# Kernel optimization log

Measured on AMD Instinct MI355X. Metric: run time of the kernel, lower is better.

## Reference

```python
import jax, jax.numpy as jnp
import numpy as np

D_IN, D, H, NL, DFF = 128, 256, 4, 4, 1024
N, B, L = 32768, 64, 672


def setup_inputs() -> dict:
    key = jax.random.key(0)
    ks = jax.random.split(key, 12)
    s = 0.02
    return {
        "dom_embeddings": jax.random.normal(ks[0], (N, D_IN), jnp.float32),
        "dom_to_event_idx": jax.random.randint(ks[1], (N,), 0, B, jnp.int32),
        "batch_size": B,
        "seq_len": L,
        "proj_w": jax.random.normal(ks[2], (D_IN, D), jnp.float32) * s,
        "proj_b": jnp.zeros((D,), jnp.float32),
        "cls_token": jax.random.normal(ks[3], (D,), jnp.float32),
        "ln1_g": jnp.ones((NL, D), jnp.float32),
        "ln1_b": jnp.zeros((NL, D), jnp.float32),
        "qkv_w": jax.random.normal(ks[4], (NL, D, 3 * D), jnp.float32) * s,
        "qkv_b": jnp.zeros((NL, 3 * D), jnp.float32),
        "out_w": jax.random.normal(ks[5], (NL, D, D), jnp.float32) * s,
        "out_b": jnp.zeros((NL, D), jnp.float32),
        "ln2_g": jnp.ones((NL, D), jnp.float32),
        "ln2_b": jnp.zeros((NL, D), jnp.float32),
        "ff1_w": jax.random.normal(ks[6], (NL, D, DFF), jnp.float32) * s,
        "ff1_b": jnp.zeros((NL, DFF), jnp.float32),
        "ff2_w": jax.random.normal(ks[7], (NL, DFF, D), jnp.float32) * s,
        "ff2_b": jnp.zeros((NL, D), jnp.float32),
        "head1_w": jax.random.normal(ks[8], (D, D), jnp.float32) * s,
        "head1_b": jnp.zeros((D,), jnp.float32),
        "head2_w": jax.random.normal(ks[9], (D, 3), jnp.float32) * s,
        "head2_b": jnp.zeros((3,), jnp.float32),
    }


def _ln(x, g, b):
    m = jnp.mean(x, axis=-1, keepdims=True)
    v = jnp.var(x, axis=-1, keepdims=True)
    return (x - m) / jnp.sqrt(v + 1e-5) * g + b


def _forward(dom_embeddings, proj_w, proj_b, cls_token, ln1_g, ln1_b, qkv_w, qkv_b,
             out_w, out_b, ln2_g, ln2_b, ff1_w, ff1_b, ff2_w, ff2_b,
             head1_w, head1_b, head2_w, head2_b, idx, batch_size, seq_len):
    n = idx.shape[0]
    d = proj_w.shape[1]
    dh = d // H
    x = dom_embeddings @ proj_w + proj_b  # (N, d)

    # per-segment rank (replaces the python for-loop): stable argsort + cumsum of counts
    counts = jnp.zeros((batch_size,), jnp.int32).at[idx].add(1)
    starts = jnp.cumsum(counts) - counts
    order = jnp.argsort(idx)  # jax sort is stable -> preserves in-event order
    rank_sorted = jnp.arange(n, dtype=jnp.int32) - starts[idx[order]]
    positions = jnp.zeros((n,), jnp.int32).at[order].set(rank_sorted)

    # scatter into padded batch; slot 0 is cls (note: cls KEY stays masked, as in torch code)
    bt = jnp.zeros((batch_size, seq_len, d), x.dtype).at[:, 0, :].set(cls_token)
    bt = bt.at[idx, positions + 1].set(x)
    pad = jnp.ones((batch_size, seq_len), bool).at[idx, positions + 1].set(False)
    bias = jnp.where(pad, -jnp.inf, 0.0).astype(x.dtype)[:, None, None, :]  # (B,1,1,L)

    h = bt
    for i in range(NL):  # norm_first pre-LN encoder layers
        y = _ln(h, ln1_g[i], ln1_b[i])
        qkv = y @ qkv_w[i] + qkv_b[i]
        q, k, v = jnp.split(qkv, 3, axis=-1)
        q = q.reshape(batch_size, seq_len, H, dh)
        k = k.reshape(batch_size, seq_len, H, dh)
        v = v.reshape(batch_size, seq_len, H, dh)
        scores = jnp.einsum('bqhd,bkhd->bhqk', q, k) * (1.0 / np.sqrt(dh))
        attn = jax.nn.softmax(scores + bias, axis=-1)
        o = jnp.einsum('bhqk,bkhd->bqhd', attn, v).reshape(batch_size, seq_len, d)
        h = h + o @ out_w[i] + out_b[i]
        z = _ln(h, ln2_g[i], ln2_b[i])
        h = h + jax.nn.relu(z @ ff1_w[i] + ff1_b[i]) @ ff2_w[i] + ff2_b[i]

    cls = h[:, 0, :]
    p = jax.nn.relu(cls @ head1_w + head1_b) @ head2_w + head2_b
    return p / jnp.sqrt(jnp.sum(p * p, axis=1, keepdims=True))


def reference(dom_embeddings, dom_to_event_idx, batch_size, seq_len, proj_w, proj_b,
              cls_token, ln1_g, ln1_b, qkv_w, qkv_b, out_w, out_b, ln2_g, ln2_b,
              ff1_w, ff1_b, ff2_w, ff2_b, head1_w, head1_b, head2_w, head2_b):
    return _forward(dom_embeddings, proj_w, proj_b, cls_token, ln1_g, ln1_b, qkv_w,
                    qkv_b, out_w, out_b, ln2_g, ln2_b, ff1_w, ff1_b, ff2_w, ff2_b,
                    head1_w, head1_b, head2_w, head2_b,
                    dom_to_event_idx, batch_size, seq_len)
```

## Files before the change

kernel.cpp:

```cpp
#include <hip/hip_runtime.h>
#include <cstdint>
#include <cstddef>

#define NDOM   32768
#define DIN    128
#define DMODEL 256
#define NHEAD  4
#define NLAYER 4
#define DFFN   1024
#define BATCH  64
#define SEQ    672
#define DHEAD  64
#define MROWS  (BATCH*SEQ)

typedef unsigned short u16;
typedef __attribute__((ext_vector_type(8))) short bf8;
typedef __attribute__((ext_vector_type(4))) float f4;

__device__ inline u16 f2b(float x) {
    union { float f; unsigned u; } c; c.f = x;
    unsigned r = c.u + 0x7fffu + ((c.u >> 16) & 1u);
    return (u16)(r >> 16);
}

__device__ inline void gload16(const void* g, const void* l) {
    __builtin_amdgcn_global_load_lds(
        (const __attribute__((address_space(1))) void*)g,
        (__attribute__((address_space(3))) void*)l, 16, 0, 0);
}


__global__ void k_zero_counts(int* __restrict__ counts) {
    if (threadIdx.x < BATCH) counts[threadIdx.x] = 0;
}

__global__ void k_pos(const int* __restrict__ idx, int* __restrict__ counts,
                      int* __restrict__ pos) {
    int i = blockIdx.x * blockDim.x + threadIdx.x;
    if (i < NDOM) pos[i] = atomicAdd(&counts[idx[i]], 1);
}

__global__ void k_init_h(float* __restrict__ h, const float* __restrict__ cls) {
    const float4* cls4 = (const float4*)cls;
    float4* h4 = (float4*)h;
    const int total4 = MROWS * DMODEL / 4;
    for (int f = blockIdx.x * blockDim.x + threadIdx.x; f < total4;
         f += gridDim.x * blockDim.x) {
        int d4 = f & 63;
        int t  = (f >> 6) % SEQ;
        h4[f] = (t == 0) ? cls4[d4] : make_float4(0.f, 0.f, 0.f, 0.f);
    }
}

__global__ void k_b16(const float* __restrict__ x, u16* __restrict__ y, int n4) {
    int i = blockIdx.x * 256 + threadIdx.x;
    if (i < n4) {
        float4 v = ((const float4*)x)[i];
        ushort4 o;
        o.x = f2b(v.x); o.y = f2b(v.y); o.z = f2b(v.z); o.w = f2b(v.w);
        ((ushort4*)y)[i] = o;
    }
}

__global__ __launch_bounds__(256) void k_wt_all(
    const float* __restrict__ projw, const float* __restrict__ qkvw,
    const float* __restrict__ outw,  const float* __restrict__ ff1w,
    const float* __restrict__ ff2w,
    u16* __restrict__ wpj, u16* __restrict__ wq, u16* __restrict__ wo,
    u16* __restrict__ w1,  u16* __restrict__ w2)
{
    __shared__ float t[64][65];
    const int tile = blockIdx.x;
    const float* W; u16* D; int K, N, local;
    if (tile < 8)        { W = projw; D = wpj; K = 128;  N = 256;  local = tile; }
    else if (tile < 200) { int l = (tile-8)/48;   local = (tile-8)%48;
                           W = qkvw + (size_t)l*196608; D = wq + (size_t)l*196608; K = 256;  N = 768; }
    else if (tile < 264) { int l = (tile-200)/16; local = (tile-200)%16;
                           W = outw + (size_t)l*65536;  D = wo + (size_t)l*65536;  K = 256;  N = 256; }
    else if (tile < 520) { int l = (tile-264)/64; local = (tile-264)%64;
                           W = ff1w + (size_t)l*262144; D = w1 + (size_t)l*262144; K = 256;  N = 1024; }
    else                 { int l = (tile-520)/64; local = (tile-520)%64;
                           W = ff2w + (size_t)l*262144; D = w2 + (size_t)l*262144; K = 1024; N = 256; }
    const int ntn = N >> 6;
    const int tk = local / ntn, tn = local % ntn;
    const int r = threadIdx.x >> 6, c = threadIdx.x & 63;
    #pragma unroll 4
    for (int rr = r; rr < 64; rr += 4)
        t[rr][c] = W[(size_t)(tk*64 + rr) * N + tn*64 + c];
    __syncthreads();
    #pragma unroll 4
    for (int rr = r; rr < 64; rr += 4)
        D[(size_t)(tn*64 + rr) * K + tk*64 + c] = f2b(t[c][rr]);
}

__global__ __launch_bounds__(256) void k_scatter(
    const float* __restrict__ xp, const int* __restrict__ idx,
    const int* __restrict__ pos, float* __restrict__ h)
{
    const int i = blockIdx.x * 4 + (threadIdx.x >> 6);
    const int lane = threadIdx.x & 63;
    const int p = pos[i] + 1;
    if (p >= SEQ) return;
    const size_t row = (size_t)idx[i] * SEQ + p;
    ((float4*)(h + row * DMODEL))[lane] = ((const float4*)(xp + (size_t)i * DMODEL))[lane];
}


__global__ __launch_bounds__(256) void k_ln_bf(
    const float* __restrict__ x, const float* __restrict__ g,
    const float* __restrict__ bt, u16* __restrict__ y)
{
    const int row  = blockIdx.x * 4 + (threadIdx.x >> 6);
    const int lane = threadIdx.x & 63;
    float4 v = ((const float4*)(x + (size_t)row * DMODEL))[lane];
    float s = v.x + v.y + v.z + v.w;
    #pragma unroll
    for (int off = 32; off >= 1; off >>= 1) s += __shfl_xor(s, off);
    const float m = s * (1.f / DMODEL);
    const float d0 = v.x - m, d1 = v.y - m, d2 = v.z - m, d3 = v.w - m;
    float q = d0*d0 + d1*d1 + d2*d2 + d3*d3;
    #pragma unroll
    for (int off = 32; off >= 1; off >>= 1) q += __shfl_xor(q, off);
    const float rstd = rsqrtf(q * (1.f / DMODEL) + 1e-5f);
    const float4 gv = ((const float4*)g)[lane];
    const float4 bv = ((const float4*)bt)[lane];
    ushort4 o;
    o.x = f2b(d0 * rstd * gv.x + bv.x);
    o.y = f2b(d1 * rstd * gv.y + bv.y);
    o.z = f2b(d2 * rstd * gv.z + bv.z);
    o.w = f2b(d3 * rstd * gv.w + bv.w);
    ((ushort4*)(y + (size_t)row * DMODEL))[lane] = o;
}


template<int RELU, int RESID, int OBF, int OF32>
__global__ __launch_bounds__(256) void k_gemm_bf(
    const u16* __restrict__ A, const u16* __restrict__ Bt,
    const float* __restrict__ bias, float* __restrict__ Cf,
    u16* __restrict__ Cb, int K, int N)
{
    __shared__ u16 As[8192];
    __shared__ u16 Bs[8192];
    const int tid = threadIdx.x;
    const int w = tid >> 6, lane = tid & 63;
    const int lr = lane & 15, lg = lane >> 4;
    const int m0 = blockIdx.y * 128, n0 = blockIdx.x * 128;
    const int wm = (w >> 1) * 64, wn = (w & 1) * 64;

    const f4 zf = {0.f, 0.f, 0.f, 0.f};
    f4 acc[4][4];
    #pragma unroll
    for (int i = 0; i < 4; ++i)
        #pragma unroll
        for (int j = 0; j < 4; ++j) acc[i][j] = zf;

    const int srow8 = lane >> 3;
    const int sq = lane & 7;

    for (int k0 = 0; k0 < K; k0 += 64) {
        #pragma unroll
        for (int c = 0; c < 4; ++c) {
            const int chunk = w * 4 + c;
            const int row = chunk * 8 + srow8;
            const int ks = k0 + ((sq ^ (row & 7)) << 3);
            gload16(A  + (size_t)(m0 + row) * K + ks, (const char*)As + chunk * 1024);
            gload16(Bt + (size_t)(n0 + row) * K + ks, (const char*)Bs + chunk * 1024);
        }
        __syncthreads();
        #pragma unroll
        for (int kk = 0; kk < 2; ++kk) {
            bf8 af[4], bg[4];
            #pragma unroll
            for (int f = 0; f < 4; ++f) {
                const int ra = wm + f * 16 + lr;
                af[f] = *(const bf8*)((const char*)As + ra * 128 +
                        ((((kk << 2) | lg) ^ (ra & 7)) << 4));
                const int rb = wn + f * 16 + lr;
                bg[f] = *(const bf8*)((const char*)Bs + rb * 128 +
                        ((((kk << 2) | lg) ^ (rb & 7)) << 4));
            }
            #pragma unroll
            for (int fm = 0; fm < 4; ++fm)
                #pragma unroll
                for (int fn = 0; fn < 4; ++fn)
                    acc[fm][fn] = __builtin_amdgcn_mfma_f32_16x16x32_bf16(
                        af[fm], bg[fn], acc[fm][fn], 0, 0, 0);
        }
        __syncthreads();
    }

    float bv[4];
    #pragma unroll
    for (int fn = 0; fn < 4; ++fn) bv[fn] = bias[n0 + wn + fn * 16 + lr];
    #pragma unroll
    for (int fm = 0; fm < 4; ++fm)
        #pragma unroll
        for (int j = 0; j < 4; ++j) {
            const int row = m0 + wm + fm * 16 + lg * 4 + j;
            #pragma unroll
            for (int fn = 0; fn < 4; ++fn) {
                float v = acc[fm][fn][j] + bv[fn];
                if (RELU) v = fmaxf(v, 0.f);
                const size_t off = (size_t)row * N + n0 + wn + fn * 16 + lr;
                if (RESID) Cf[off] += v;
                if (OF32)  Cf[off] = v;
                if (OBF)   Cb[off] = f2b(v);
            }
        }
}


__global__ __launch_bounds__(256) void k_attn_mfma(
    const u16* __restrict__ qkv, const int* __restrict__ counts,
    u16* __restrict__ out)
{
    __shared__ u16 Ks[4096];
    __shared__ u16 Vt[4096];
    __shared__ u16 Ps[4][1024];
    const int tid = threadIdx.x;
    const int w = tid >> 6, lane = tid & 63;
    const int lr = lane & 15, lg = lane >> 4;
    const int b = blockIdx.z, hh = blockIdx.y;
    const int q0 = blockIdx.x * 64;
    const int kmax = min(counts[b], SEQ - 1);
    if (q0 > kmax) return;
    const int ntiles = (kmax + 64) >> 6;
    const size_t bb = (size_t)b * SEQ;

    const int qrow = q0 + w * 16 + lr;
    const size_t qoff = (bb + (size_t)min(qrow, SEQ - 1)) * 768 + hh * 64 + (lg << 3);
    const bf8 qf0 = *(const bf8*)(qkv + qoff);
    const bf8 qf1 = *(const bf8*)(qkv + qoff + 32);

    const f4 zf = {0.f, 0.f, 0.f, 0.f};
    f4 o_[4];
    #pragma unroll
    for (int fn = 0; fn < 4; ++fn) o_[fn] = zf;
    float mrow = -INFINITY, ssum = 0.f;

    for (int kt = 0; kt < ntiles; ++kt) {
        const int k0 = kt * 64;
        #pragma unroll
        for (int c = 0; c < 2; ++c) {
            const int chunk = w * 2 + c;
            const int row = chunk * 8 + (lane >> 3);
            const int q = lane & 7;
            const int krow = min(k0 + row, SEQ - 1);
            gload16(qkv + (bb + krow) * 768 + 256 + hh * 64 + ((q ^ (row & 7)) << 3),
                    (const char*)Ks + chunk * 1024);
        }
        {
            const int kk2 = (tid & 31) * 2;
            const int dh0 = (tid >> 5) * 8;
            const int r0 = min(k0 + kk2, SEQ - 1), r1 = min(k0 + kk2 + 1, SEQ - 1);
            const bf8 v0 = *(const bf8*)(qkv + (bb + r0) * 768 + 512 + hh * 64 + dh0);
            const bf8 v1 = *(const bf8*)(qkv + (bb + r1) * 768 + 512 + hh * 64 + dh0);
            #pragma unroll
            for (int e = 0; e < 8; ++e) {
                const int d = dh0 + e;
                const unsigned pk = (unsigned)(u16)v0[e] | ((unsigned)(u16)v1[e] << 16);
                *(unsigned*)((char*)Vt + d * 128 +
                    ((((kk2 >> 3) ^ (d & 7)) << 4)) + ((kk2 & 7) << 1)) = pk;
            }
        }
        __syncthreads();

        f4 sf[4];
        #pragma unroll
        for (int fk = 0; fk < 4; ++fk) sf[fk] = zf;
        #pragma unroll
        for (int kk = 0; kk < 2; ++kk) {
            const bf8 qf = kk ? qf1 : qf0;
            #pragma unroll
            for (int fk = 0; fk < 4; ++fk) {
                const int rk = fk * 16 + lr;
                const bf8 kf = *(const bf8*)((const char*)Ks + rk * 128 +
                        ((((kk << 2) | lg) ^ (rk & 7)) << 4));
                sf[fk] = __builtin_amdgcn_mfma_f32_16x16x32_bf16(kf, qf, sf[fk], 0, 0, 0);
            }
        }

        float sv[4][4];
        float pmax = -INFINITY;
        #pragma unroll
        for (int fk = 0; fk < 4; ++fk)
            #pragma unroll
            for (int j = 0; j < 4; ++j) {
                const int key = k0 + fk * 16 + lg * 4 + j;
                float x = (key >= 1 && key <= kmax) ? sf[fk][j] * 0.125f : -INFINITY;
                sv[fk][j] = x;
                pmax = fmaxf(pmax, x);
            }
        pmax = fmaxf(pmax, __shfl_xor(pmax, 16));
        pmax = fmaxf(pmax, __shfl_xor(pmax, 32));
        const float mnew = fmaxf(mrow, pmax);
        const float fac = __expf(mrow - mnew);
        mrow = mnew;
        float tsum = 0.f;
        #pragma unroll
        for (int fk = 0; fk < 4; ++fk) {
            const float p0 = __expf(sv[fk][0] - mnew);
            const float p1 = __expf(sv[fk][1] - mnew);
            const float p2 = __expf(sv[fk][2] - mnew);
            const float p3 = __expf(sv[fk][3] - mnew);
            tsum += p0 + p1 + p2 + p3;
            ushort4 pk;
            pk.x = f2b(p0); pk.y = f2b(p1); pk.z = f2b(p2); pk.w = f2b(p3);
            *(ushort4*)((char*)Ps[w] + lr * 128 +
                (((((fk << 1) | (lg >> 1)) ^ (lr & 7)) << 4)) + ((lg & 1) << 3)) = pk;
        }
        tsum += __shfl_xor(tsum, 16);
        tsum += __shfl_xor(tsum, 32);
        ssum = ssum * fac + tsum;

        #pragma unroll
        for (int j = 0; j < 4; ++j) {
            const float fj = __shfl(fac, lg * 4 + j);
            #pragma unroll
            for (int fn = 0; fn < 4; ++fn) o_[fn][j] *= fj;
        }
        __syncthreads();

        #pragma unroll
        for (int kk = 0; kk < 2; ++kk) {
            const bf8 pa = *(const bf8*)((const char*)Ps[w] + lr * 128 +
                    ((((kk << 2) | lg) ^ (lr & 7)) << 4));
            #pragma unroll
            for (int fn = 0; fn < 4; ++fn) {
                const int rv = fn * 16 + lr;
                const bf8 vf = *(const bf8*)((const char*)Vt + rv * 128 +
                        ((((kk << 2) | lg) ^ (rv & 7)) << 4));
                o_[fn] = __builtin_amdgcn_mfma_f32_16x16x32_bf16(pa, vf, o_[fn], 0, 0, 0);
            }
        }
        __syncthreads();
    }

    const float inv = 1.f / ssum;
    #pragma unroll
    for (int j = 0; j < 4; ++j) {
        const float ij = __shfl(inv, lg * 4 + j);
        const int qr = q0 + w * 16 + lg * 4 + j;
        if (qr < SEQ) {
            #pragma unroll
            for (int fn = 0; fn < 4; ++fn)
                out[(bb + qr) * DMODEL + hh * 64 + fn * 16 + lr] = f2b(o_[fn][j] * ij);
        }
    }
}


__global__ __launch_bounds__(256) void k_head(
    const float* __restrict__ h, const float* __restrict__ w1,
    const float* __restrict__ b1, const float* __restrict__ w2,
    const float* __restrict__ b2, float* __restrict__ out)
{
    __shared__ float cbuf[DMODEL];
    __shared__ float p1[DMODEL];
    __shared__ float p2[3];
    const int b = blockIdx.x, tid = threadIdx.x;
    cbuf[tid] = h[(size_t)b * SEQ * DMODEL + tid];
    __syncthreads();
    float acc = b1[tid];
    #pragma unroll 8
    for (int k = 0; k < DMODEL; ++k) acc = fmaf(cbuf[k], w1[k * DMODEL + tid], acc);
    p1[tid] = fmaxf(acc, 0.f);
    __syncthreads();
    if (tid < 3) {
        float a = b2[tid];
        for (int k = 0; k < DMODEL; ++k) a = fmaf(p1[k], w2[k * 3 + tid], a);
        p2[tid] = a;
    }
    __syncthreads();
    if (tid < 3) {
        float n2 = p2[0]*p2[0] + p2[1]*p2[1] + p2[2]*p2[2];
        out[b * 3 + tid] = p2[tid] * rsqrtf(n2);
    }
}


extern "C" void kernel_launch(void* const* d_in, const int* in_sizes, int n_in,
                              void* d_out, int out_size, void* d_ws, size_t ws_size,
                              hipStream_t stream) {
    const float* emb   = (const float*)d_in[0];
    const int*   idx   = (const int*)d_in[1];
    const float* projw = (const float*)d_in[4];
    const float* projb = (const float*)d_in[5];
    const float* cls   = (const float*)d_in[6];
    const float* ln1g  = (const float*)d_in[7];
    const float* ln1b  = (const float*)d_in[8];
    const float* qkvw  = (const float*)d_in[9];
    const float* qkvb  = (const float*)d_in[10];
    const float* outw  = (const float*)d_in[11];
    const float* outb  = (const float*)d_in[12];
    const float* ln2g  = (const float*)d_in[13];
    const float* ln2b  = (const float*)d_in[14];
    const float* ff1w  = (const float*)d_in[15];
    const float* ff1b  = (const float*)d_in[16];
    const float* ff2w  = (const float*)d_in[17];
    const float* ff2b  = (const float*)d_in[18];
    const float* h1w   = (const float*)d_in[19];
    const float* h1b   = (const float*)d_in[20];
    const float* h2w   = (const float*)d_in[21];
    const float* h2b   = (const float*)d_in[22];
    float* out = (float*)d_out;

    char* ws = (char*)d_ws;
    int*   counts = (int*)ws;
    int*   pos    = (int*)(ws + 4096);
    float* h      = (float*)(ws + 135168);
    u16*   ybf    = (u16*)(ws + 44175360);
    u16*   qkvb16 = (u16*)(ws + 66195456);
    u16*   ffb    = (u16*)(ws + 132354048);
    u16*   wq     = (u16*)(ws + 220434432);
    u16*   wo     = (u16*)(ws + 222007296);
    u16*   w1     = (u16*)(ws + 222531584);
    u16*   w2     = (u16*)(ws + 224628736);
    u16*   wpj    = (u16*)(ws + 226725888);
    u16*   embbf  = qkvb16;
    float* xp     = (float*)ffb;

    k_zero_counts<<<1, 64, 0, stream>>>(counts);
    k_pos<<<NDOM / 256, 256, 0, stream>>>(idx, counts, pos);
    k_b16<<<(NDOM * DIN / 4) / 256, 256, 0, stream>>>(emb, embbf, NDOM * DIN / 4);
    k_wt_all<<<776, 256, 0, stream>>>(projw, qkvw, outw, ff1w, ff2w,
                                      wpj, wq, wo, w1, w2);
    k_init_h<<<2688, 256, 0, stream>>>(h, cls);
    k_gemm_bf<0,0,0,1><<<dim3(2, 256), 256, 0, stream>>>(
        embbf, wpj, projb, xp, nullptr, DIN, DMODEL);
    k_scatter<<<NDOM / 4, 256, 0, stream>>>(xp, idx, pos, h);

    for (int l = 0; l < NLAYER; ++l) {
        k_ln_bf<<<MROWS / 4, 256, 0, stream>>>(h, ln1g + l * DMODEL, ln1b + l * DMODEL, ybf);
        k_gemm_bf<0,0,1,0><<<dim3(6, 336), 256, 0, stream>>>(
            ybf, wq + (size_t)l * 196608, qkvb + l * 768, nullptr, qkvb16, 256, 768);
        k_attn_mfma<<<dim3(11, NHEAD, BATCH), 256, 0, stream>>>(qkvb16, counts, ybf);
        k_gemm_bf<0,1,0,0><<<dim3(2, 336), 256, 0, stream>>>(
            ybf, wo + (size_t)l * 65536, outb + l * DMODEL, h, nullptr, 256, 256);
        k_ln_bf<<<MROWS / 4, 256, 0, stream>>>(h, ln2g + l * DMODEL, ln2b + l * DMODEL, ybf);
        k_gemm_bf<1,0,1,0><<<dim3(8, 336), 256, 0, stream>>>(
            ybf, w1 + (size_t)l * 262144, ff1b + l * DFFN, nullptr, ffb, 256, 1024);
        k_gemm_bf<0,1,0,0><<<dim3(2, 336), 256, 0, stream>>>(
            ffb, w2 + (size_t)l * 262144, ff2b + l * DMODEL, h, nullptr, 1024, 256);
    }

    k_head<<<BATCH, 256, 0, stream>>>(h, h1w, h1b, h2w, h2b, out);
}
```

Measured before the change: 1.166 ms.

## Fuse residual GEMMs with following LayerNorm and retile attention to 128-query blocks

Adds a full-row (128x256) GEMM kernel that applies the bias and residual add and then computes the next LayerNorm in its epilogue, writing both h and the bf16 normalized input. This removes the separate LN kernels and their extra reads of h. Attention now uses 512-thread blocks covering 128 queries, with a flattened grid remapped so batches interleave across blocks. It also adds a fast path that skips masking on fully valid key tiles. The risks are lower occupancy, since each full-row block is large and uses more shared memory, and fewer, larger GEMM blocks.

Result: no change. 1.184 ms (+1.6%).

```diff
diff --git a/kernel.cpp b/kernel.cpp
--- a/kernel.cpp
+++ b/kernel.cpp
@@ -210,18 +210,163 @@
 }
 
 
-__global__ __launch_bounds__(256) void k_attn_mfma(
+template<int LNF>
+__global__ __launch_bounds__(512) void k_gemm_ln(
+    const u16* __restrict__ A, const u16* __restrict__ Bt,
+    const float* __restrict__ bias, float* __restrict__ h,
+    u16* __restrict__ ybf, const float* __restrict__ lng,
+    const float* __restrict__ lnb, int K)
+{
+    __shared__ u16 As[8192];
+    __shared__ u16 Bs[16384];
+    __shared__ float red[8][136];
+    const int tid = threadIdx.x;
+    const int w = tid >> 6, lane = tid & 63;
+    const int lr = lane & 15, lg = lane >> 4;
+    const int m0 = blockIdx.x * 128;
+    const int wm = (w >> 2) * 64, wn = (w & 3) * 64;
+
+    const f4 zf = {0.f, 0.f, 0.f, 0.f};
+    f4 acc[4][4];
+    #pragma unroll
+    for (int i = 0; i < 4; ++i)
+        #pragma unroll
+        for (int j = 0; j < 4; ++j) acc[i][j] = zf;
+
+    const int srow8 = lane >> 3;
+    const int sq = lane & 7;
+
+    for (int k0 = 0; k0 < K; k0 += 64) {
+        #pragma unroll
+        for (int c = 0; c < 2; ++c) {
+            const int chunk = w * 2 + c;
+            const int row = chunk * 8 + srow8;
+            const int ks = k0 + ((sq ^ (row & 7)) << 3);
+            gload16(A + (size_t)(m0 + row) * K + ks, (const char*)As + chunk * 1024);
+        }
+        #pragma unroll
+        for (int c = 0; c < 4; ++c) {
+            const int chunk = w * 4 + c;
+            const int row = chunk * 8 + srow8;
+            const int ks = k0 + ((sq ^ (row & 7)) << 3);
+            gload16(Bt + (size_t)row * K + ks, (const char*)Bs + chunk * 1024);
+        }
+        __syncthreads();
+        #pragma unroll
+        for (int kk = 0; kk < 2; ++kk) {
+            bf8 af[4], bg[4];
+            #pragma unroll
+            for (int f = 0; f < 4; ++f) {
+                const int ra = wm + f * 16 + lr;
+                af[f] = *(const bf8*)((const char*)As + ra * 128 +
+                        ((((kk << 2) | lg) ^ (ra & 7)) << 4));
+                const int rb = wn + f * 16 + lr;
+                bg[f] = *(const bf8*)((const char*)Bs + rb * 128 +
+                        ((((kk << 2) | lg) ^ (rb & 7)) << 4));
+            }
+            #pragma unroll
+            for (int fm = 0; fm < 4; ++fm)
+                #pragma unroll
+                for (int fn = 0; fn < 4; ++fn)
+                    acc[fm][fn] = __builtin_amdgcn_mfma_f32_16x16x32_bf16(
+                        af[fm], bg[fn], acc[fm][fn], 0, 0, 0);
+        }
+        __syncthreads();
+    }
+
+    float bv[4];
+    #pragma unroll
+    for (int fn = 0; fn < 4; ++fn) bv[fn] = bias[wn + fn * 16 + lr];
+    float sr[4][4], s2r[4][4];
+    #pragma unroll
+    for (int fm = 0; fm < 4; ++fm)
+        #pragma unroll
+        for (int j = 0; j < 4; ++j) {
+            const int row = m0 + wm + fm * 16 + lg * 4 + j;
+            float s = 0.f, s2 = 0.f;
+            #pragma unroll
+            for (int fn = 0; fn < 4; ++fn) {
+                float v = acc[fm][fn][j] + bv[fn];
+                v += h[(size_t)row * DMODEL + wn + fn * 16 + lr];
+                acc[fm][fn][j] = v;
+                s += v; s2 += v * v;
+            }
+            if (LNF) {
+                #pragma unroll
+                for (int off = 1; off <= 8; off <<= 1) {
+                    s  += __shfl_xor(s, off);
+                    s2 += __shfl_xor(s2, off);
+                }
+            }
+            sr[fm][j] = s; s2r[fm][j] = s2;
+        }
+
+    if (LNF) {
+        if (lr == 0) {
+            #pragma unroll
+            for (int fm = 0; fm < 4; ++fm)
+                #pragma unroll
+                for (int j = 0; j < 4; ++j) {
+                    const int rL = wm + fm * 16 + lg * 4 + j;
+                    red[(w & 3) * 2 + 0][rL] = sr[fm][j];
+                    red[(w & 3) * 2 + 1][rL] = s2r[fm][j];
+                }
+        }
+        __syncthreads();
+        float gl[4], bl[4];
+        #pragma unroll
+        for (int fn = 0; fn < 4; ++fn) {
+            gl[fn] = lng[wn + fn * 16 + lr];
+            bl[fn] = lnb[wn + fn * 16 + lr];
+        }
+        #pragma unroll
+        for (int fm = 0; fm < 4; ++fm)
+            #pragma unroll
+            for (int j = 0; j < 4; ++j) {
+                const int rL = wm + fm * 16 + lg * 4 + j;
+                const int row = m0 + rL;
+                const float S  = red[0][rL] + red[2][rL] + red[4][rL] + red[6][rL];
+                const float S2 = red[1][rL] + red[3][rL] + red[5][rL] + red[7][rL];
+                const float mean = S * (1.f / DMODEL);
+                const float var  = S2 * (1.f / DMODEL) - mean * mean;
+                const float rstd = rsqrtf(var + 1e-5f);
+                #pragma unroll
+                for (int fn = 0; fn < 4; ++fn) {
+                    const float v = acc[fm][fn][j];
+                    const size_t off = (size_t)row * DMODEL + wn + fn * 16 + lr;
+                    h[off] = v;
+                    ybf[off] = f2b((v - mean) * rstd * gl[fn] + bl[fn]);
+                }
+            }
+    } else {
+        #pragma unroll
+        for (int fm = 0; fm < 4; ++fm)
+            #pragma unroll
+            for (int j = 0; j < 4; ++j) {
+                const int row = m0 + wm + fm * 16 + lg * 4 + j;
+                #pragma unroll
+                for (int fn = 0; fn < 4; ++fn)
+                    h[(size_t)row * DMODEL + wn + fn * 16 + lr] = acc[fm][fn][j];
+            }
+    }
+}
+
+
+__global__ __launch_bounds__(512) void k_attn_mfma(
     const u16* __restrict__ qkv, const int* __restrict__ counts,
     u16* __restrict__ out)
 {
     __shared__ u16 Ks[4096];
     __shared__ u16 Vt[4096];
-    __shared__ u16 Ps[4][1024];
+    __shared__ u16 Ps[8][1024];
     const int tid = threadIdx.x;
     const int w = tid >> 6, lane = tid & 63;
     const int lr = lane & 15, lg = lane >> 4;
-    const int b = blockIdx.z, hh = blockIdx.y;
-    const int q0 = blockIdx.x * 64;
+    const int L = blockIdx.x;
+    const int b = (L & 7) * 8 + (L >> 3) / 24;
+    const int r = (L >> 3) % 24;
+    const int qt = r >> 2, hh = r & 3;
+    const int q0 = qt * 128;
     const int kmax = min(counts[b], SEQ - 1);
     if (q0 > kmax) return;
     const int ntiles = (kmax + 64) >> 6;
@@ -240,25 +385,25 @@
 
     for (int kt = 0; kt < ntiles; ++kt) {
         const int k0 = kt * 64;
-        #pragma unroll
-        for (int c = 0; c < 2; ++c) {
-            const int chunk = w * 2 + c;
-            const int row = chunk * 8 + (lane >> 3);
+        {
+            const int row = w * 8 + (lane >> 3);
             const int q = lane & 7;
             const int krow = min(k0 + row, SEQ - 1);
             gload16(qkv + (bb + krow) * 768 + 256 + hh * 64 + ((q ^ (row & 7)) << 3),
-                    (const char*)Ks + chunk * 1024);
+                    (const char*)Ks + w * 1024);
         }
         {
             const int kk2 = (tid & 31) * 2;
-            const int dh0 = (tid >> 5) * 8;
+            const int dh0 = (tid >> 5) * 4;
             const int r0 = min(k0 + kk2, SEQ - 1), r1 = min(k0 + kk2 + 1, SEQ - 1);
-            const bf8 v0 = *(const bf8*)(qkv + (bb + r0) * 768 + 512 + hh * 64 + dh0);
-            const bf8 v1 = *(const bf8*)(qkv + (bb + r1) * 768 + 512 + hh * 64 + dh0);
-            #pragma unroll
-            for (int e = 0; e < 8; ++e) {
+            const ushort4 v0 = *(const ushort4*)(qkv + (bb + r0) * 768 + 512 + hh * 64 + dh0);
+            const ushort4 v1 = *(const ushort4*)(qkv + (bb + r1) * 768 + 512 + hh * 64 + dh0);
+            const u16* pv0 = (const u16*)&v0;
+            const u16* pv1 = (const u16*)&v1;
+            #pragma unroll
+            for (int e = 0; e < 4; ++e) {
                 const int d = dh0 + e;
-                const unsigned pk = (unsigned)(u16)v0[e] | ((unsigned)(u16)v1[e] << 16);
+                const unsigned pk = (unsigned)pv0[e] | ((unsigned)pv1[e] << 16);
                 *(unsigned*)((char*)Vt + d * 128 +
                     ((((kk2 >> 3) ^ (d & 7)) << 4)) + ((kk2 & 7) << 1)) = pk;
             }
@@ -282,15 +427,26 @@
 
         float sv[4][4];
         float pmax = -INFINITY;
-        #pragma unroll
-        for (int fk = 0; fk < 4; ++fk)
-            #pragma unroll
-            for (int j = 0; j < 4; ++j) {
-                const int key = k0 + fk * 16 + lg * 4 + j;
-                float x = (key >= 1 && key <= kmax) ? sf[fk][j] * 0.125f : -INFINITY;
-                sv[fk][j] = x;
-                pmax = fmaxf(pmax, x);
-            }
+        if (k0 >= 1 && k0 + 63 <= kmax) {
+            #pragma unroll
+            for (int fk = 0; fk < 4; ++fk)
+                #pragma unroll
+                for (int j = 0; j < 4; ++j) {
+                    const float x = sf[fk][j] * 0.125f;
+                    sv[fk][j] = x;
+                    pmax = fmaxf(pmax, x);
+                }
+        } else {
+            #pragma unroll
+            for (int fk = 0; fk < 4; ++fk)
+                #pragma unroll
+                for (int j = 0; j < 4; ++j) {
+                    const int key = k0 + fk * 16 + lg * 4 + j;
+                    const float x = (key >= 1 && key <= kmax) ? sf[fk][j] * 0.125f : -INFINITY;
+                    sv[fk][j] = x;
+                    pmax = fmaxf(pmax, x);
+                }
+        }
         pmax = fmaxf(pmax, __shfl_xor(pmax, 16));
         pmax = fmaxf(pmax, __shfl_xor(pmax, 32));
         const float mnew = fmaxf(mrow, pmax);
@@ -429,19 +585,25 @@
     k_gemm_bf<0,0,0,1><<<dim3(2, 256), 256, 0, stream>>>(
         embbf, wpj, projb, xp, nullptr, DIN, DMODEL);
     k_scatter<<<NDOM / 4, 256, 0, stream>>>(xp, idx, pos, h);
+    k_ln_bf<<<MROWS / 4, 256, 0, stream>>>(h, ln1g, ln1b, ybf);
 
     for (int l = 0; l < NLAYER; ++l) {
-        k_ln_bf<<<MROWS / 4, 256, 0, stream>>>(h, ln1g + l * DMODEL, ln1b + l * DMODEL, ybf);
         k_gemm_bf<0,0,1,0><<<dim3(6, 336), 256, 0, stream>>>(
             ybf, wq + (size_t)l * 196608, qkvb + l * 768, nullptr, qkvb16, 256, 768);
-        k_attn_mfma<<<dim3(11, NHEAD, BATCH), 256, 0, stream>>>(qkvb16, counts, ybf);
-        k_gemm_bf<0,1,0,0><<<dim3(2, 336), 256, 0, stream>>>(
-            ybf, wo + (size_t)l * 65536, outb + l * DMODEL, h, nullptr, 256, 256);
-        k_ln_bf<<<MROWS / 4, 256, 0, stream>>>(h, ln2g + l * DMODEL, ln2b + l * DMODEL, ybf);
+        k_attn_mfma<<<1536, 512, 0, stream>>>(qkvb16, counts, ybf);
+        k_gemm_ln<1><<<336, 512, 0, stream>>>(
+            ybf, wo + (size_t)l * 65536, outb + l * DMODEL, h, ybf,
+            ln2g + l * DMODEL, ln2b + l * DMODEL, 256);
         k_gemm_bf<1,0,1,0><<<dim3(8, 336), 256, 0, stream>>>(
             ybf, w1 + (size_t)l * 262144, ff1b + l * DFFN, nullptr, ffb, 256, 1024);
-        k_gemm_bf<0,1,0,0><<<dim3(2, 336), 256, 0, stream>>>(
-            ffb, w2 + (size_t)l * 262144, ff2b + l * DMODEL, h, nullptr, 1024, 256);
+        if (l < NLAYER - 1)
+            k_gemm_ln<1><<<336, 512, 0, stream>>>(
+                ffb, w2 + (size_t)l * 262144, ff2b + l * DMODEL, h, ybf,
+                ln1g + (l + 1) * DMODEL, ln1b + (l + 1) * DMODEL, 1024);
+        else
+            k_gemm_ln<0><<<336, 512, 0, stream>>>(
+                ffb, w2 + (size_t)l * 262144, ff2b + l * DMODEL, h, nullptr,
+                nullptr, nullptr, 1024);
     }
 
     k_head<<<BATCH, 256, 0, stream>>>(h, h1w, h1b, h2w, h2b, out);
```
